# Optimization experiments

Hardware: AMD Instinct MI355X
Metric: run time of the kernel (lower is better)

Reference implementation:

```python
import jax, jax.numpy as jnp
import numpy as np

B, S, D, H, E = 4, 2048, 512, 8, 4  # batch, seq, embed, heads, expand
HD = D // H


def setup_inputs() -> dict:
    key = jax.random.key(0)
    ks = jax.random.split(key, 9)
    s = lambda k, shape, fan: jax.random.normal(k, shape, jnp.float32) * (fan ** -0.5)
    return {
        "x": jax.random.normal(ks[0], (B, S, D), jnp.float32),
        "Wq": s(ks[1], (D, D), D),
        "Wk": s(ks[2], (D, D), D),
        "Wv": s(ks[3], (D, D), D),
        "Wo": s(ks[4], (D, D), D),
        "W1": s(ks[5], (D, D * E), D),
        "b1": jnp.zeros((D * E,), jnp.float32),
        "W2": s(ks[6], (D * E, D), D * E),
        "b2": jnp.zeros((D,), jnp.float32),
    }


def _encoder_layer(x, Wq, Wk, Wv, Wo, W1, b1, W2, b2):
    # NOTE: source computes InstanceNorm1d twice but discards both results -> no-ops.
    scale = D ** -0.25  # applied to BOTH q and k (net 1/sqrt(embed_dim))
    q = (x @ Wq).reshape(B, S, H, HD).transpose(0, 2, 1, 3) * scale  # [B,H,S,hd]
    k = (x @ Wk).reshape(B, S, H, HD).transpose(0, 2, 1, 3) * scale
    v = (x @ Wv).reshape(B, S, H, HD).transpose(0, 2, 1, 3)
    scores = jnp.einsum('bhqd,bhkd->bhqk', q, k)  # [B,H,S,S]
    attn = jax.nn.softmax(scores, axis=-1)
    o = jnp.einsum('bhqk,bhkd->bhqd', attn, v)  # [B,H,S,hd]
    o = o.transpose(0, 2, 1, 3).reshape(B, S, D)
    x = o @ Wo + x  # residual 1
    h = jax.nn.gelu(x @ W1 + b1, approximate=True)  # torch GELU(approximate='tanh')
    return h @ W2 + b2 + x  # residual 2 (dropout=0, eval)


def reference(x, Wq, Wk, Wv, Wo, W1, b1, W2, b2):
    return _encoder_layer(x, Wq, Wk, Wv, Wo, W1, b1, W2, b2)
```

## Files before the change

### kernel.cpp

```cpp
#include <hip/hip_runtime.h>
#include <hip/hip_bf16.h>


typedef __bf16 bf16;
typedef __attribute__((ext_vector_type(8))) __bf16 bf16x8;
typedef __attribute__((ext_vector_type(4))) __bf16 bf16x4;
typedef __attribute__((ext_vector_type(4))) float f32x4;

#define LOG2E 1.4426950408889634f
#define SCORE_SCALE 0.044194173824159216f
#define SCALE_L2E (SCORE_SCALE * LOG2E)
#define FIXED_M 12.0f
#define PLD 70

#if __has_builtin(__builtin_amdgcn_exp2f)
#define EXP2(x) __builtin_amdgcn_exp2f(x)
#else
#define EXP2(x) exp2f(x)
#endif

__device__ __forceinline__ void gl_lds16(const bf16* g, bf16* l) {
  __builtin_amdgcn_global_load_lds(
      (const __attribute__((address_space(1))) unsigned int*)g,
      (__attribute__((address_space(3))) unsigned int*)l, 16, 0, 0);
}

__device__ __forceinline__ float gelu_tanh(float x) {
  float u = 0.7978845608028654f * (x + 0.044715f * x * x * x);
  float e = EXP2(u * (2.0f * LOG2E));
  float th = 1.0f - 2.0f / (e + 1.0f);
  return 0.5f * x * (1.0f + th);
}

__device__ __forceinline__ f32x4 mfma_bf16(bf16x8 a, bf16x8 b, f32x4 c) {
  return __builtin_amdgcn_mfma_f32_16x16x32_bf16(a, b, c, 0, 0, 0);
}

template <int MODE, typename OutT, int TN>
__global__ __launch_bounds__(256, 2) void gemm_bt(
    const bf16* __restrict__ A, const bf16* __restrict__ Bt,
    OutT* __restrict__ C, const float* __restrict__ bias,
    const float* __restrict__ resf, const bf16* __restrict__ resb,
    int M, int N, int K) {
  constexpr int MI = (TN == 128) ? 4 : 2;
  __shared__ __align__(16) bf16 sA[2][128 * 32];
  __shared__ __align__(16) bf16 sB[2][TN * 32];
  const int tid = threadIdx.x;
  const int lane = tid & 63;
  const int quad = lane >> 4, lc = lane & 15;
  const int wave = tid >> 6;
  const int wr = (TN == 128) ? (wave >> 1) : wave;
  const int wc = (TN == 128) ? (wave & 1) : 0;
  const int m0 = blockIdx.y * 128, n0 = blockIdx.x * TN;

  const int srow = tid >> 2;
  const int kc = (tid & 3) * 8;
  const bf16* Ag1 = A + (size_t)(m0 + srow) * K + kc;
  const bf16* Ag2 = A + (size_t)(m0 + 64 + srow) * K + kc;
  const bf16* Bg1 = Bt + (size_t)(n0 + srow) * K + kc;
  const bf16* Bg2 = Bt + (size_t)(n0 + 64 + srow) * K + kc;
  const int o1 = tid * 8, o2 = (tid + 256) * 8;

  f32x4 acc[MI][4];
#pragma unroll
  for (int mi = 0; mi < MI; ++mi)
#pragma unroll
    for (int ni = 0; ni < 4; ++ni) acc[mi][ni] = (f32x4){0.f, 0.f, 0.f, 0.f};

  gl_lds16(Ag1, sA[0] + o1);
  gl_lds16(Ag2, sA[0] + o2);
  gl_lds16(Bg1, sB[0] + o1);
  if (TN == 128) gl_lds16(Bg2, sB[0] + o2);
  Ag1 += 32; Ag2 += 32; Bg1 += 32; Bg2 += 32;

  const int kIters = K >> 5;
  for (int kt = 0; kt < kIters; ++kt) {
    __syncthreads();
    const bf16* cA = sA[kt & 1];
    const bf16* cB = sB[kt & 1];
    if (kt + 1 < kIters) {
      bf16* nA = sA[(kt + 1) & 1];
      bf16* nB = sB[(kt + 1) & 1];
      gl_lds16(Ag1, nA + o1);
      gl_lds16(Ag2, nA + o2);
      gl_lds16(Bg1, nB + o1);
      if (TN == 128) gl_lds16(Bg2, nB + o2);
      Ag1 += 32; Ag2 += 32; Bg1 += 32; Bg2 += 32;
    }

    bf16x8 af[MI], bfm[4];
#pragma unroll
    for (int i = 0; i < MI; ++i)
      af[i] =
          *(const bf16x8*)(cA + ((wr * (16 * MI) + i * 16 + lc) * 32 + quad * 8));
#pragma unroll
    for (int i = 0; i < 4; ++i)
      bfm[i] = *(const bf16x8*)(cB + ((wc * 64 + i * 16 + lc) * 32 + quad * 8));
#pragma unroll
    for (int mi = 0; mi < MI; ++mi)
#pragma unroll
      for (int ni = 0; ni < 4; ++ni)
        acc[mi][ni] = mfma_bf16(af[mi], bfm[ni], acc[mi][ni]);
  }

#pragma unroll
  for (int mi = 0; mi < MI; ++mi) {
#pragma unroll
    for (int r = 0; r < 4; ++r) {
      const int row = m0 + wr * (16 * MI) + mi * 16 + quad * 4 + r;
#pragma unroll
      for (int ni = 0; ni < 4; ++ni) {
        const int col = n0 + wc * 64 + ni * 16 + lc;
        const size_t idx = (size_t)row * N + col;
        float v = acc[mi][ni][r];
        if (MODE == 1) v += resf[idx];
        if (MODE == 2) v = gelu_tanh(v + bias[col]);
        if (MODE == 3) v += bias[col] + (float)resb[idx];
        C[idx] = (OutT)v;
      }
    }
  }
}

__global__ __launch_bounds__(256, 2) void flash_attn(
    const bf16* __restrict__ QKV, const bf16* __restrict__ Vt,
    bf16* __restrict__ O) {
  const int tid = threadIdx.x;
  const int lane = tid & 63, wave = tid >> 6;
  const int quad = lane >> 4, lc = lane & 15;
  const int bh = blockIdx.y, b = bh >> 3, h = bh & 7;
  const int q0 = blockIdx.x * 128;

  __shared__ __align__(16) bf16 sK[2][4096];
  __shared__ __align__(16) bf16 sV[2][4096];
  __shared__ __align__(16) bf16 sP[4][32 * PLD];
  bf16* sPw = sP[wave];

  bf16x8 qf[2][2];
#pragma unroll
  for (int s = 0; s < 2; ++s) {
    const size_t qrow =
        (size_t)(b * 2048 + q0 + wave * 32 + s * 16 + lc) * 1536 + h * 64;
    qf[s][0] = *(const bf16x8*)(QKV + qrow + quad * 8);
    qf[s][1] = *(const bf16x8*)(QKV + qrow + 32 + quad * 8);
  }

  const int colsw = (((lane & 7) ^ (lane >> 3)) << 3);
  const bf16* Kg = QKV + (size_t)b * 2048 * 1536 + 512 + (size_t)h * 64 +
                   (size_t)(wave * 16 + (lane >> 3)) * 1536 + colsw;
  const bf16* Vg = Vt + (size_t)bh * 64 * 2048 +
                   (size_t)(wave * 16 + (lane >> 3)) * 2048 + colsw;
  const int stag = wave * 1024;

  const int m7 = lc & 7;
  const int off0 = lc * 64 + ((quad ^ m7) << 3);
  const int off1 = off0 ^ 32;

  bf16x8 bones;
#pragma unroll
  for (int j = 0; j < 8; ++j) bones[j] = (lc == 0) ? (bf16)1.0f : (bf16)0.0f;

  f32x4 oacc[2][4], osum[2];
#pragma unroll
  for (int s = 0; s < 2; ++s) {
    osum[s] = (f32x4){0.f, 0.f, 0.f, 0.f};
#pragma unroll
    for (int dt = 0; dt < 4; ++dt) oacc[s][dt] = (f32x4){0.f, 0.f, 0.f, 0.f};
  }

  gl_lds16(Kg, sK[0] + stag);
  gl_lds16(Kg + 8 * 1536, sK[0] + stag + 512);
  gl_lds16(Vg, sV[0] + stag);
  gl_lds16(Vg + 8 * 2048, sV[0] + stag + 512);
  Kg += (size_t)64 * 1536;

  for (int kt = 0; kt < 32; ++kt) {
    __syncthreads();
    const bf16* cK = sK[kt & 1];
    const bf16* cV = sV[kt & 1];
    if (kt < 31) {
      bf16* nK = sK[(kt + 1) & 1];
      bf16* nV = sV[(kt + 1) & 1];
      gl_lds16(Kg, nK + stag);
      gl_lds16(Kg + 8 * 1536, nK + stag + 512);
      gl_lds16(Vg + (kt + 1) * 64, nV + stag);
      gl_lds16(Vg + (kt + 1) * 64 + 8 * 2048, nV + stag + 512);
      Kg += (size_t)64 * 1536;
    }

    f32x4 sacc[2][4];
#pragma unroll
    for (int s = 0; s < 2; ++s)
#pragma unroll
      for (int nt = 0; nt < 4; ++nt) sacc[s][nt] = (f32x4){0.f, 0.f, 0.f, 0.f};
#pragma unroll
    for (int nt = 0; nt < 4; ++nt) {
      bf16x8 k0 = *(const bf16x8*)(cK + nt * 1024 + off0);
      bf16x8 k1 = *(const bf16x8*)(cK + nt * 1024 + off1);
      sacc[0][nt] = mfma_bf16(qf[0][0], k0, sacc[0][nt]);
      sacc[0][nt] = mfma_bf16(qf[0][1], k1, sacc[0][nt]);
      sacc[1][nt] = mfma_bf16(qf[1][0], k0, sacc[1][nt]);
      sacc[1][nt] = mfma_bf16(qf[1][1], k1, sacc[1][nt]);
    }
#pragma unroll
    for (int s = 0; s < 2; ++s)
#pragma unroll
      for (int nt = 0; nt < 4; ++nt)
#pragma unroll
        for (int r = 0; r < 4; ++r) {
          float p = EXP2(sacc[s][nt][r] * SCALE_L2E - FIXED_M);
          sPw[(s * 16 + quad * 4 + r) * PLD + nt * 16 + lc] = (bf16)p;
        }
    __asm__ __volatile__("s_waitcnt lgkmcnt(0)" ::: "memory");

    bf16x8 pf[2][2];
#pragma unroll
    for (int s = 0; s < 2; ++s) {
      pf[s][0] = *(const bf16x8*)(sPw + (s * 16 + lc) * PLD + quad * 8);
      pf[s][1] = *(const bf16x8*)(sPw + (s * 16 + lc) * PLD + 32 + quad * 8);
    }
#pragma unroll
    for (int dt = 0; dt < 4; ++dt) {
      bf16x8 v0 = *(const bf16x8*)(cV + dt * 1024 + off0);
      bf16x8 v1 = *(const bf16x8*)(cV + dt * 1024 + off1);
      oacc[0][dt] = mfma_bf16(pf[0][0], v0, oacc[0][dt]);
      oacc[0][dt] = mfma_bf16(pf[0][1], v1, oacc[0][dt]);
      oacc[1][dt] = mfma_bf16(pf[1][0], v0, oacc[1][dt]);
      oacc[1][dt] = mfma_bf16(pf[1][1], v1, oacc[1][dt]);
    }
#pragma unroll
    for (int s = 0; s < 2; ++s) {
      osum[s] = mfma_bf16(pf[s][0], bones, osum[s]);
      osum[s] = mfma_bf16(pf[s][1], bones, osum[s]);
    }
  }

#pragma unroll
  for (int s = 0; s < 2; ++s) {
    const size_t obase =
        (size_t)(b * 2048 + q0 + wave * 32 + s * 16) * 512 + h * 64;
#pragma unroll
    for (int r = 0; r < 4; ++r) {
      const float sumv = __shfl(osum[s][r], (lane & 48), 64);
      const float inv = 1.0f / sumv;
#pragma unroll
      for (int dt = 0; dt < 4; ++dt)
        O[obase + (size_t)(quad * 4 + r) * 512 + dt * 16 + lc] =
            (bf16)(oacc[s][dt][r] * inv);
    }
  }
}

__global__ __launch_bounds__(256) void prep(
    const float* __restrict__ x, const float* __restrict__ Wq,
    const float* __restrict__ Wk, const float* __restrict__ Wv,
    const float* __restrict__ Wo, const float* __restrict__ W1,
    const float* __restrict__ W2, bf16* __restrict__ xb,
    bf16* __restrict__ WqkvT, bf16* __restrict__ WoT, bf16* __restrict__ W1T,
    bf16* __restrict__ W2T) {
  const int bid = blockIdx.x;
  if (bid < 4096) {
    const size_t i = ((size_t)bid * 256 + threadIdx.x) * 4;
    const float4 v = *(const float4*)(x + i);
    bf16x4 o;
    o[0] = (bf16)v.x; o[1] = (bf16)v.y; o[2] = (bf16)v.z; o[3] = (bf16)v.w;
    *(bf16x4*)(xb + i) = o;
    return;
  }
  const int t = bid - 4096;
  const float* in;
  bf16* out;
  int in_ld, out_ld, bx, by;
  if (t < 1024) {
    const int q = t >> 8, r = t & 255;
    bx = r & 15; by = r >> 4; in_ld = 512; out_ld = 512;
    in = (q == 0) ? Wq : (q == 1) ? Wk : (q == 2) ? Wv : Wo;
    out = (q == 0) ? WqkvT
          : (q == 1) ? WqkvT + 512 * 512
          : (q == 2) ? WqkvT + 2 * 512 * 512
                     : WoT;
  } else if (t < 2048) {
    const int r = t - 1024;
    bx = r & 63; by = r >> 6; in_ld = 2048; out_ld = 512;
    in = W1; out = W1T;
  } else {
    const int r = t - 2048;
    bx = r & 15; by = r >> 4; in_ld = 512; out_ld = 2048;
    in = W2; out = W2T;
  }
  __shared__ __align__(16) bf16 tl[32][33];
  const int tx = threadIdx.x & 31, ty = threadIdx.x >> 5;
  const int n0 = bx * 32, k0 = by * 32;
#pragma unroll
  for (int i = 0; i < 4; ++i)
    tl[ty + 8 * i][tx] = (bf16)in[(size_t)(k0 + ty + 8 * i) * in_ld + n0 + tx];
  __syncthreads();
#pragma unroll
  for (int i = 0; i < 4; ++i)
    out[(size_t)(n0 + ty + 8 * i) * out_ld + k0 + tx] = tl[tx][ty + 8 * i];
}

__global__ __launch_bounds__(256) void transpose_v(
    const bf16* __restrict__ QKV, bf16* __restrict__ Vt) {
  __shared__ __align__(16) bf16 t[32][33];
  const int tx = threadIdx.x & 31, ty = threadIdx.x >> 5;
  const int bh = blockIdx.z, b = bh >> 3, h = bh & 7;
  const bf16* ip = QKV + (size_t)b * 2048 * 1536 + 1024 + h * 64;
  bf16* op = Vt + (size_t)bh * 64 * 2048;
  const int d0 = blockIdx.x * 32, s0 = blockIdx.y * 32;
#pragma unroll
  for (int i = 0; i < 4; ++i)
    t[ty + 8 * i][tx] = ip[(size_t)(s0 + ty + 8 * i) * 1536 + d0 + tx];
  __syncthreads();
#pragma unroll
  for (int i = 0; i < 4; ++i)
    op[(size_t)(d0 + ty + 8 * i) * 2048 + s0 + tx] = t[tx][ty + 8 * i];
}

extern "C" void kernel_launch(void* const* d_in, const int* in_sizes, int n_in,
                              void* d_out, int out_size, void* d_ws,
                              size_t ws_size, hipStream_t stream) {
  const float* x = (const float*)d_in[0];
  const float* Wq = (const float*)d_in[1];
  const float* Wk = (const float*)d_in[2];
  const float* Wv = (const float*)d_in[3];
  const float* Wo = (const float*)d_in[4];
  const float* W1 = (const float*)d_in[5];
  const float* b1 = (const float*)d_in[6];
  const float* W2 = (const float*)d_in[7];
  const float* b2 = (const float*)d_in[8];
  float* out = (float*)d_out;

  char* ws = (char*)d_ws;
  size_t off = 0;
  auto alloc = [&](size_t bytes) {
    char* p = ws + off;
    off += (bytes + 255) & ~(size_t)255;
    return p;
  };
  bf16* WqkvT = (bf16*)alloc(1536ULL * 512 * 2);
  bf16* WoT = (bf16*)alloc(512ULL * 512 * 2);
  bf16* W1T = (bf16*)alloc(2048ULL * 512 * 2);
  bf16* W2T = (bf16*)alloc(512ULL * 2048 * 2);
  bf16* xb = (bf16*)alloc(8192ULL * 512 * 2);
  bf16* QKV = (bf16*)alloc(8192ULL * 1536 * 2);
  bf16* Vt = (bf16*)alloc(32ULL * 64 * 2048 * 2);
  bf16* attn = (bf16*)alloc(8192ULL * 512 * 2);
  bf16* x2 = xb;
  bf16* hbuf = QKV;

  const dim3 tb(256);
  prep<<<dim3(7168), tb, 0, stream>>>(x, Wq, Wk, Wv, Wo, W1, W2, xb, WqkvT,
                                      WoT, W1T, W2T);
  gemm_bt<0, bf16, 128><<<dim3(12, 64), tb, 0, stream>>>(
      xb, WqkvT, QKV, nullptr, nullptr, nullptr, 8192, 1536, 512);
  transpose_v<<<dim3(2, 64, 32), tb, 0, stream>>>(QKV, Vt);
  flash_attn<<<dim3(16, 32), tb, 0, stream>>>(QKV, Vt, attn);
  gemm_bt<1, bf16, 64><<<dim3(8, 64), tb, 0, stream>>>(
      attn, WoT, x2, nullptr, x, nullptr, 8192, 512, 512);
  gemm_bt<2, bf16, 128><<<dim3(16, 64), tb, 0, stream>>>(
      x2, W1T, hbuf, b1, nullptr, nullptr, 8192, 2048, 512);
  gemm_bt<3, float, 64><<<dim3(8, 64), tb, 0, stream>>>(
      hbuf, W2T, out, b2, nullptr, x2, 8192, 512, 2048);
}
```

Baseline: 286.8 us.

## Rewrite flash attention with 32x32 MFMA and register-resident P

Switches the attention kernel from 16x16x32 MFMA tiles to 32x32 MFMA, computing S transposed (K as the A operand) so each lane holds a column of probabilities. Those probabilities feed the PV product directly from registers through 32x32x8 MFMA, which removes the per-wave LDS staging buffer for P and its extra waitcnt. The row sum is now accumulated in VALU and combined with a cross-lane shuffle, replacing the extra MFMA against a ones vector. The risks are higher register pressure and different LDS access patterns for K and V.

```diff
diff --git a/kernel.cpp b/kernel.cpp
--- a/kernel.cpp
+++ b/kernel.cpp
@@ -6,12 +6,13 @@
 typedef __attribute__((ext_vector_type(8))) __bf16 bf16x8;
 typedef __attribute__((ext_vector_type(4))) __bf16 bf16x4;
 typedef __attribute__((ext_vector_type(4))) float f32x4;
+typedef __attribute__((ext_vector_type(16))) float f32x16;
+typedef __attribute__((ext_vector_type(4))) short s16x4;
 
 #define LOG2E 1.4426950408889634f
 #define SCORE_SCALE 0.044194173824159216f
 #define SCALE_L2E (SCORE_SCALE * LOG2E)
 #define FIXED_M 12.0f
-#define PLD 70
 
 #if __has_builtin(__builtin_amdgcn_exp2f)
 #define EXP2(x) __builtin_amdgcn_exp2f(x)
@@ -34,6 +35,17 @@
 
 __device__ __forceinline__ f32x4 mfma_bf16(bf16x8 a, bf16x8 b, f32x4 c) {
   return __builtin_amdgcn_mfma_f32_16x16x32_bf16(a, b, c, 0, 0, 0);
+}
+__device__ __forceinline__ f32x16 mfma32x16(bf16x8 a, bf16x8 b, f32x16 c) {
+  return __builtin_amdgcn_mfma_f32_32x32x16_bf16(a, b, c, 0, 0, 0);
+}
+__device__ __forceinline__ f32x16 mfma32x8(bf16x4 a, bf16x4 b, f32x16 c) {
+#if __has_builtin(__builtin_amdgcn_mfma_f32_32x32x8_bf16)
+  return __builtin_amdgcn_mfma_f32_32x32x8_bf16(a, b, c, 0, 0, 0);
+#else
+  return __builtin_amdgcn_mfma_f32_32x32x8bf16_1k(
+      __builtin_bit_cast(s16x4, a), __builtin_bit_cast(s16x4, b), c, 0, 0, 0);
+#endif
 }
 
 template <int MODE, typename OutT, int TN>
@@ -127,23 +139,17 @@
     bf16* __restrict__ O) {
   const int tid = threadIdx.x;
   const int lane = tid & 63, wave = tid >> 6;
-  const int quad = lane >> 4, lc = lane & 15;
+  const int lo5 = lane & 31, hi = lane >> 5;
   const int bh = blockIdx.y, b = bh >> 3, h = bh & 7;
-  const int q0 = blockIdx.x * 128;
+  const int q0 = blockIdx.x * 128 + wave * 32;
 
   __shared__ __align__(16) bf16 sK[2][4096];
   __shared__ __align__(16) bf16 sV[2][4096];
-  __shared__ __align__(16) bf16 sP[4][32 * PLD];
-  bf16* sPw = sP[wave];
-
-  bf16x8 qf[2][2];
-#pragma unroll
-  for (int s = 0; s < 2; ++s) {
-    const size_t qrow =
-        (size_t)(b * 2048 + q0 + wave * 32 + s * 16 + lc) * 1536 + h * 64;
-    qf[s][0] = *(const bf16x8*)(QKV + qrow + quad * 8);
-    qf[s][1] = *(const bf16x8*)(QKV + qrow + 32 + quad * 8);
-  }
+
+  const bf16* Qrow = QKV + (size_t)(b * 2048 + q0 + lo5) * 1536 + h * 64;
+  bf16x8 qf[4];
+#pragma unroll
+  for (int i = 0; i < 4; ++i) qf[i] = *(const bf16x8*)(Qrow + i * 16 + hi * 8);
 
   const int colsw = (((lane & 7) ^ (lane >> 3)) << 3);
   const bf16* Kg = QKV + (size_t)b * 2048 * 1536 + 512 + (size_t)h * 64 +
@@ -152,21 +158,12 @@
                    (size_t)(wave * 16 + (lane >> 3)) * 2048 + colsw;
   const int stag = wave * 1024;
 
-  const int m7 = lc & 7;
-  const int off0 = lc * 64 + ((quad ^ m7) << 3);
-  const int off1 = off0 ^ 32;
-
-  bf16x8 bones;
-#pragma unroll
-  for (int j = 0; j < 8; ++j) bones[j] = (lc == 0) ? (bf16)1.0f : (bf16)0.0f;
-
-  f32x4 oacc[2][4], osum[2];
-#pragma unroll
-  for (int s = 0; s < 2; ++s) {
-    osum[s] = (f32x4){0.f, 0.f, 0.f, 0.f};
-#pragma unroll
-    for (int dt = 0; dt < 4; ++dt) oacc[s][dt] = (f32x4){0.f, 0.f, 0.f, 0.f};
-  }
+  const int m7 = lo5 & 7;
+
+  f32x16 oacc[2];
+  oacc[0] = (f32x16)(0.f);
+  oacc[1] = (f32x16)(0.f);
+  float rsum = 0.f;
 
   gl_lds16(Kg, sK[0] + stag);
   gl_lds16(Kg + 8 * 1536, sK[0] + stag + 512);
@@ -188,66 +185,52 @@
       Kg += (size_t)64 * 1536;
     }
 
-    f32x4 sacc[2][4];
-#pragma unroll
-    for (int s = 0; s < 2; ++s)
-#pragma unroll
-      for (int nt = 0; nt < 4; ++nt) sacc[s][nt] = (f32x4){0.f, 0.f, 0.f, 0.f};
-#pragma unroll
-    for (int nt = 0; nt < 4; ++nt) {
-      bf16x8 k0 = *(const bf16x8*)(cK + nt * 1024 + off0);
-      bf16x8 k1 = *(const bf16x8*)(cK + nt * 1024 + off1);
-      sacc[0][nt] = mfma_bf16(qf[0][0], k0, sacc[0][nt]);
-      sacc[0][nt] = mfma_bf16(qf[0][1], k1, sacc[0][nt]);
-      sacc[1][nt] = mfma_bf16(qf[1][0], k0, sacc[1][nt]);
-      sacc[1][nt] = mfma_bf16(qf[1][1], k1, sacc[1][nt]);
-    }
-#pragma unroll
-    for (int s = 0; s < 2; ++s)
-#pragma unroll
-      for (int nt = 0; nt < 4; ++nt)
-#pragma unroll
-        for (int r = 0; r < 4; ++r) {
-          float p = EXP2(sacc[s][nt][r] * SCALE_L2E - FIXED_M);
-          sPw[(s * 16 + quad * 4 + r) * PLD + nt * 16 + lc] = (bf16)p;
+    bf16x4 pa[2][4];
+#pragma unroll
+    for (int hl = 0; hl < 2; ++hl) {
+      f32x16 st = (f32x16)(0.f);
+#pragma unroll
+      for (int i = 0; i < 4; ++i) {
+        const int R = hl * 32 + lo5;
+        bf16x8 kf =
+            *(const bf16x8*)(cK + R * 64 + (((2 * i + hi) ^ m7) << 3));
+        st = mfma32x16(kf, qf[i], st);
+      }
+#pragma unroll
+      for (int g = 0; g < 4; ++g) {
+        bf16x4 pb;
+#pragma unroll
+        for (int j = 0; j < 4; ++j) {
+          float p = EXP2(st[4 * g + j] * SCALE_L2E - FIXED_M);
+          rsum += p;
+          pb[j] = (bf16)p;
         }
-    __asm__ __volatile__("s_waitcnt lgkmcnt(0)" ::: "memory");
-
-    bf16x8 pf[2][2];
-#pragma unroll
-    for (int s = 0; s < 2; ++s) {
-      pf[s][0] = *(const bf16x8*)(sPw + (s * 16 + lc) * PLD + quad * 8);
-      pf[s][1] = *(const bf16x8*)(sPw + (s * 16 + lc) * PLD + 32 + quad * 8);
-    }
-#pragma unroll
-    for (int dt = 0; dt < 4; ++dt) {
-      bf16x8 v0 = *(const bf16x8*)(cV + dt * 1024 + off0);
-      bf16x8 v1 = *(const bf16x8*)(cV + dt * 1024 + off1);
-      oacc[0][dt] = mfma_bf16(pf[0][0], v0, oacc[0][dt]);
-      oacc[0][dt] = mfma_bf16(pf[0][1], v1, oacc[0][dt]);
-      oacc[1][dt] = mfma_bf16(pf[1][0], v0, oacc[1][dt]);
-      oacc[1][dt] = mfma_bf16(pf[1][1], v1, oacc[1][dt]);
-    }
-#pragma unroll
-    for (int s = 0; s < 2; ++s) {
-      osum[s] = mfma_bf16(pf[s][0], bones, osum[s]);
-      osum[s] = mfma_bf16(pf[s][1], bones, osum[s]);
-    }
-  }
-
-#pragma unroll
-  for (int s = 0; s < 2; ++s) {
-    const size_t obase =
-        (size_t)(b * 2048 + q0 + wave * 32 + s * 16) * 512 + h * 64;
-#pragma unroll
-    for (int r = 0; r < 4; ++r) {
-      const float sumv = __shfl(osum[s][r], (lane & 48), 64);
-      const float inv = 1.0f / sumv;
-#pragma unroll
-      for (int dt = 0; dt < 4; ++dt)
-        O[obase + (size_t)(quad * 4 + r) * 512 + dt * 16 + lc] =
-            (bf16)(oacc[s][dt][r] * inv);
-    }
+        pa[hl][g] = pb;
+      }
+    }
+
+#pragma unroll
+    for (int dh = 0; dh < 2; ++dh) {
+      const int Rd = dh * 32 + lo5;
+#pragma unroll
+      for (int ks = 0; ks < 8; ++ks) {
+        bf16x4 vf =
+            *(const bf16x4*)(cV + Rd * 64 + (((ks ^ m7)) << 3) + hi * 4);
+        oacc[dh] = mfma32x8(pa[ks >> 2][ks & 3], vf, oacc[dh]);
+      }
+    }
+  }
+
+  rsum += __shfl_xor(rsum, 32, 64);
+  const size_t obase = (size_t)(b * 2048 + q0) * 512 + h * 64;
+#pragma unroll
+  for (int r = 0; r < 16; ++r) {
+    const int qloc = (r & 3) + 8 * (r >> 2) + 4 * hi;
+    const float inv = 1.0f / __shfl(rsum, qloc, 64);
+#pragma unroll
+    for (int dh = 0; dh < 2; ++dh)
+      O[obase + (size_t)qloc * 512 + dh * 32 + lo5] =
+          (bf16)(oacc[dh][r] * inv);
   }
 }
 
```

Result: faster. 264.9 us (-7.6%).
